# Kernel tuning notes

Measured on AMD Instinct MI355X. Metric: run time of the kernel, lower is better.

## Reference

```python
import jax, jax.numpy as jnp
import numpy as np

N = 50000      # n_nodes
E = 800000     # n_edges (avg degree 16)
D_IN, D_HID, D_OUT = 128, 128, 64


def setup_inputs() -> dict:
    key = jax.random.key(0)
    k1, k2, k3, k4 = jax.random.split(key, 4)
    x = jax.random.normal(k1, (N, D_IN), jnp.float32)
    edge_index = jax.random.randint(k2, (2, E), 0, N, jnp.int32)
    # Glorot-style init for the two GCNConv linear weights
    W1 = jax.random.normal(k3, (D_IN, D_HID), jnp.float32) / np.sqrt(D_IN)
    W2 = jax.random.normal(k4, (D_HID, D_OUT), jnp.float32) / np.sqrt(D_HID)
    b1 = jnp.zeros((D_HID,), jnp.float32)
    b2 = jnp.zeros((D_OUT,), jnp.float32)
    return {"x": x, "edge_index": edge_index, "W1": W1, "b1": b1, "W2": W2, "b2": b2}


def _gcn_conv(x, W, b, src, dst):
    """PyG GCNConv: linear transform, then sym-normalized aggregation with self-loops."""
    h = x @ W                                   # [N, F_out]
    ones = jnp.ones((src.shape[0],), h.dtype)
    # degree includes the self-loop weight of 1
    deg = jax.ops.segment_sum(ones, dst, num_segments=N) + 1.0
    dinv = jax.lax.rsqrt(deg)                   # D^{-1/2}
    norm = dinv[src] * dinv[dst]                # per-edge normalization
    agg = jax.ops.segment_sum(h[src] * norm[:, None], dst, num_segments=N)
    # self-loop contribution: norm_ii = dinv_i^2
    return agg + h * (dinv * dinv)[:, None] + b


def reference(x, edge_index, W1, b1, W2, b2):
    src, dst = edge_index[0], edge_index[1]
    h = jax.nn.relu(_gcn_conv(x, W1, b1, src, dst))
    out = jax.nn.relu(_gcn_conv(h, W2, b2, src, dst))
    return out
```

## Files before the change

### kernel.cpp

```cpp
#include <hip/hip_runtime.h>

typedef unsigned short u16;
typedef __attribute__((ext_vector_type(8))) short short8;
typedef __attribute__((ext_vector_type(4))) float f32x4;

__device__ __forceinline__ float bflo(unsigned u) {
    union { unsigned u; float f; } v; v.u = u << 16; return v.f;
}
__device__ __forceinline__ float bfhi(unsigned u) {
    union { unsigned u; float f; } v; v.u = u & 0xFFFF0000u; return v.f;
}
__device__ __forceinline__ u16 f2bf(float f) {
    union { float f; unsigned u; } v; v.f = f;
    unsigned u = v.u;
    u += 0x7FFFu + ((u >> 16) & 1u);
    return (u16)(u >> 16);
}

__global__ void k_deg_detect(const int* __restrict__ dst, int* __restrict__ cnt,
                             int* __restrict__ pos, int E,
                             const u16* __restrict__ x, int* __restrict__ flag) {
    if (blockIdx.x == 0) {
        __shared__ int c_s;
        if (threadIdx.x == 0) c_s = 0;
        __syncthreads();
        int c = 0;
        for (int i = threadIdx.x; i < 2048; i += 256) {
            int ex = (x[2 * i] >> 7) & 0xFF;
            c += (ex >= 160 || ex <= 80) ? 1 : 0;
        }
        atomicAdd(&c_s, c);
        __syncthreads();
        if (threadIdx.x == 0) *flag = (c_s > 64) ? 1 : 0;
    }
    int e = blockIdx.x * 256 + threadIdx.x;
    if (e < E) pos[e] = atomicAdd(&cnt[dst[e]], 1);
}

__global__ void k_scan(const int* __restrict__ cnt, int* __restrict__ rowp,
                       float* __restrict__ dinv, int n, int E, int nb) {
    __shared__ int S[256];
    __shared__ int T[256];
    int t = threadIdx.x;
    int b = blockIdx.x;
    int s = 0;
    if (t < nb) {
        const int4* p4 = (const int4*)(cnt + t * 256);
#pragma unroll 8
        for (int i = 0; i < 64; i++) { int4 v = p4[i]; s += v.x + v.y + v.z + v.w; }
    }
    S[t] = s;
    __syncthreads();
    for (int off = 1; off < 256; off <<= 1) {
        int add = (t >= off) ? S[t - off] : 0;
        __syncthreads();
        S[t] += add;
        __syncthreads();
    }
    int prefix = (b == 0) ? 0 : S[b - 1];
    int i = b * 256 + t;
    int v = (i < n) ? cnt[i] : 0;
    T[t] = v;
    __syncthreads();
    for (int off = 1; off < 256; off <<= 1) {
        int add = (t >= off) ? T[t - off] : 0;
        __syncthreads();
        T[t] += add;
        __syncthreads();
    }
    if (i < n) {
        rowp[i] = prefix + T[t] - v;
        dinv[i] = rsqrtf((float)v + 1.0f);
    }
    if (i == 0) rowp[n] = E;
}

__global__ void k_gemm1_fill(const void* __restrict__ Av, const void* __restrict__ W,
                             const float* __restrict__ dinv, u16* __restrict__ out,
                             int M, int GB, const int* __restrict__ flag,
                             const int* __restrict__ src, const int* __restrict__ dst,
                             const int* __restrict__ pos, const int* __restrict__ rowp,
                             int* __restrict__ col, int E) {
    constexpr int NOUT = 128;
    int t = threadIdx.x;
    if ((int)blockIdx.x >= GB) {
        int stride = (gridDim.x - GB) * 256;
        for (int e = ((int)blockIdx.x - GB) * 256 + t; e < E; e += stride)
            col[rowp[dst[e]] + pos[e]] = src[e];
        return;
    }
    int fl = *flag;
    __shared__ u16 Wt[NOUT][136];
    for (int idx = t; idx < NOUT * 128; idx += 256) {
        int k = idx / NOUT, n = idx % NOUT;
        Wt[n][k] = fl ? f2bf(((const float*)W)[idx]) : ((const u16*)W)[idx];
    }
    __syncthreads();
    int wave = t >> 6, lane = t & 63;
    int m0 = ((int)blockIdx.x * 4 + wave) * 16;
    if (m0 >= M) return;
    int q = lane >> 4;
    int mr = lane & 15;

    short8 a[4];
    if (fl) {
        const float* arow = (const float*)Av + (size_t)(m0 + mr) * 128 + q * 8;
#pragma unroll
        for (int c = 0; c < 4; c++) {
            f32x4 lo = *(const f32x4*)(arow + c * 32);
            f32x4 hi = *(const f32x4*)(arow + c * 32 + 4);
            a[c][0] = (short)f2bf(lo.x); a[c][1] = (short)f2bf(lo.y);
            a[c][2] = (short)f2bf(lo.z); a[c][3] = (short)f2bf(lo.w);
            a[c][4] = (short)f2bf(hi.x); a[c][5] = (short)f2bf(hi.y);
            a[c][6] = (short)f2bf(hi.z); a[c][7] = (short)f2bf(hi.w);
        }
    } else {
        const u16* arow = (const u16*)Av + (size_t)(m0 + mr) * 128 + q * 8;
#pragma unroll
        for (int c = 0; c < 4; c++) a[c] = *(const short8*)(arow + c * 32);
    }

    f32x4 acc[NOUT / 16];
#pragma unroll
    for (int tl = 0; tl < NOUT / 16; tl++) acc[tl] = (f32x4){0.f, 0.f, 0.f, 0.f};
#pragma unroll
    for (int c = 0; c < 4; c++) {
#pragma unroll
        for (int tl = 0; tl < NOUT / 16; tl++) {
            short8 b = *(const short8*)(&Wt[tl * 16 + mr][c * 32 + q * 8]);
            acc[tl] = __builtin_amdgcn_mfma_f32_16x16x32_bf16(a[c], b, acc[tl], 0, 0, 0);
        }
    }
    int rbase = m0 + q * 4;
#pragma unroll
    for (int tl = 0; tl < NOUT / 16; tl++) {
#pragma unroll
        for (int r = 0; r < 4; r++) {
            int row = rbase + r;
            float v = acc[tl][r] * dinv[row];
            out[(size_t)row * NOUT + tl * 16 + mr] = f2bf(v);
        }
    }
}

template <int NOUT>
__global__ void k_gemm_scale(const u16* __restrict__ A, const void* __restrict__ W,
                             const float* __restrict__ dinv, u16* __restrict__ out,
                             int M, const int* __restrict__ flag) {
    int fl = *flag;
    __shared__ u16 Wt[NOUT][136];
    int t = threadIdx.x;
    for (int idx = t; idx < NOUT * 128; idx += 256) {
        int k = idx / NOUT, n = idx % NOUT;
        Wt[n][k] = fl ? f2bf(((const float*)W)[idx]) : ((const u16*)W)[idx];
    }
    __syncthreads();
    int wave = t >> 6, lane = t & 63;
    int m0 = ((int)blockIdx.x * 4 + wave) * 16;
    if (m0 >= M) return;
    int q = lane >> 4;
    int mr = lane & 15;

    const u16* arow = A + (size_t)(m0 + mr) * 128 + q * 8;
    short8 a[4];
#pragma unroll
    for (int c = 0; c < 4; c++) a[c] = *(const short8*)(arow + c * 32);

    f32x4 acc[NOUT / 16];
#pragma unroll
    for (int tl = 0; tl < NOUT / 16; tl++) acc[tl] = (f32x4){0.f, 0.f, 0.f, 0.f};
#pragma unroll
    for (int c = 0; c < 4; c++) {
#pragma unroll
        for (int tl = 0; tl < NOUT / 16; tl++) {
            short8 b = *(const short8*)(&Wt[tl * 16 + mr][c * 32 + q * 8]);
            acc[tl] = __builtin_amdgcn_mfma_f32_16x16x32_bf16(a[c], b, acc[tl], 0, 0, 0);
        }
    }
    int rbase = m0 + q * 4;
#pragma unroll
    for (int tl = 0; tl < NOUT / 16; tl++) {
#pragma unroll
        for (int r = 0; r < 4; r++) {
            int row = rbase + r;
            float v = acc[tl][r] * dinv[row];
            out[(size_t)row * NOUT + tl * 16 + mr] = f2bf(v);
        }
    }
}

template <int F>
__global__ void k_agg(const u16* __restrict__ g, const int* __restrict__ rowp,
                      const int* __restrict__ col, const float* __restrict__ dinv,
                      const void* __restrict__ biasv, u16* __restrict__ outh,
                      float* __restrict__ outf, const int* __restrict__ flag,
                      int outsel, int N, int E) {
    constexpr int LPR = F / 8;
    constexpr int EPW = 64 / LPR;
    int d = blockIdx.x * 4 + (threadIdx.x >> 6);
    if (d >= N) return;
    int lane = threadIdx.x & 63;
    int er = lane / LPR;
    int fo = (lane % LPR) * 8;

    int beg = rowp[d], end = rowp[d + 1];
    if (beg < 0) beg = 0;
    if (end > E) end = E;
    int deg = end - beg;

    float a0[8], a1[8];
#pragma unroll
    for (int j = 0; j < 8; j++) { a0[j] = 0.f; a1[j] = 0.f; }

    for (int base = 0; base < deg; base += 64) {
        int cnt = deg - base; if (cnt > 64) cnt = 64;
        int colv = 0;
        if (lane < cnt) {
            int s = col[beg + base + lane];
            colv = s < 0 ? 0 : (s >= N ? N - 1 : s);
        }
        int full = cnt / EPW;
        int i = 0;
        for (; i + 2 <= full; i += 2) {
            int s0 = __shfl(colv, i * EPW + er, 64);
            int s1 = __shfl(colv, (i + 1) * EPW + er, 64);
            uint4 v0 = *(const uint4*)(g + (size_t)s0 * F + fo);
            uint4 v1 = *(const uint4*)(g + (size_t)s1 * F + fo);
            a0[0] += bflo(v0.x); a0[1] += bfhi(v0.x);
            a0[2] += bflo(v0.y); a0[3] += bfhi(v0.y);
            a0[4] += bflo(v0.z); a0[5] += bfhi(v0.z);
            a0[6] += bflo(v0.w); a0[7] += bfhi(v0.w);
            a1[0] += bflo(v1.x); a1[1] += bfhi(v1.x);
            a1[2] += bflo(v1.y); a1[3] += bfhi(v1.y);
            a1[4] += bflo(v1.z); a1[5] += bfhi(v1.z);
            a1[6] += bflo(v1.w); a1[7] += bfhi(v1.w);
        }
        if (i < full) {
            int s0 = __shfl(colv, i * EPW + er, 64);
            uint4 v0 = *(const uint4*)(g + (size_t)s0 * F + fo);
            a0[0] += bflo(v0.x); a0[1] += bfhi(v0.x);
            a0[2] += bflo(v0.y); a0[3] += bfhi(v0.y);
            a0[4] += bflo(v0.z); a0[5] += bfhi(v0.z);
            a0[6] += bflo(v0.w); a0[7] += bfhi(v0.w);
            i++;
        }
        int rem = cnt - full * EPW;
        int s0 = __shfl(colv, (full * EPW + er) & 63, 64);
        if (er < rem) {
            uint4 v0 = *(const uint4*)(g + (size_t)s0 * F + fo);
            a0[0] += bflo(v0.x); a0[1] += bfhi(v0.x);
            a0[2] += bflo(v0.y); a0[3] += bfhi(v0.y);
            a0[4] += bflo(v0.z); a0[5] += bfhi(v0.z);
            a0[6] += bflo(v0.w); a0[7] += bfhi(v0.w);
        }
    }
#pragma unroll
    for (int j = 0; j < 8; j++) a0[j] += a1[j];
#pragma unroll
    for (int off = LPR; off < 64; off <<= 1) {
#pragma unroll
        for (int j = 0; j < 8; j++) a0[j] += __shfl_xor(a0[j], off, 64);
    }

    if (lane < LPR) {
        int fl = *flag;
        uint4 sv = *(const uint4*)(g + (size_t)d * F + fo);
        float bb[8];
        if (fl) {
            const float* bp = (const float*)biasv + fo;
            f32x4 blo = *(const f32x4*)bp;
            f32x4 bhi = *(const f32x4*)(bp + 4);
            bb[0] = blo.x; bb[1] = blo.y; bb[2] = blo.z; bb[3] = blo.w;
            bb[4] = bhi.x; bb[5] = bhi.y; bb[6] = bhi.z; bb[7] = bhi.w;
        } else {
            uint4 bv = *(const uint4*)((const u16*)biasv + fo);
            bb[0] = bflo(bv.x); bb[1] = bfhi(bv.x);
            bb[2] = bflo(bv.y); bb[3] = bfhi(bv.y);
            bb[4] = bflo(bv.z); bb[5] = bfhi(bv.z);
            bb[6] = bflo(bv.w); bb[7] = bfhi(bv.w);
        }
        float di = dinv[d];
        float sf[8] = { bflo(sv.x), bfhi(sv.x), bflo(sv.y), bfhi(sv.y),
                        bflo(sv.z), bfhi(sv.z), bflo(sv.w), bfhi(sv.w) };
        float r[8];
#pragma unroll
        for (int j = 0; j < 8; j++) {
            float v = di * (a0[j] + sf[j]) + bb[j];
            r[j] = v > 0.f ? v : 0.f;
        }
        size_t o = (size_t)d * F + fo;
        if (outsel && fl) {
            f32x4 w0 = {r[0], r[1], r[2], r[3]};
            f32x4 w1 = {r[4], r[5], r[6], r[7]};
            *(f32x4*)(outf + o) = w0;
            *(f32x4*)(outf + o + 4) = w1;
        } else {
            uint4 w;
            w.x = (unsigned)f2bf(r[0]) | ((unsigned)f2bf(r[1]) << 16);
            w.y = (unsigned)f2bf(r[2]) | ((unsigned)f2bf(r[3]) << 16);
            w.z = (unsigned)f2bf(r[4]) | ((unsigned)f2bf(r[5]) << 16);
            w.w = (unsigned)f2bf(r[6]) | ((unsigned)f2bf(r[7]) << 16);
            *(uint4*)(outh + o) = w;
        }
    }
}


extern "C" void kernel_launch(void* const* d_in, const int* in_sizes, int n_in,
                              void* d_out, int out_size, void* d_ws, size_t ws_size,
                              hipStream_t stream) {
    const int N = in_sizes[0] / 128;
    const int E = in_sizes[1] / 2;
    const int* ei = (const int*)d_in[1];
    const int* src = ei;
    const int* dst = ei + E;

    char* p = (char*)d_ws;
    auto alloc = [&](size_t b) { char* r = p; p += (b + 255) & ~(size_t)255; return r; };
    int*   flag = (int*)alloc(256);
    int*   rowp = (int*)alloc((size_t)(N + 1) * 4);
    float* dinv = (float*)alloc((size_t)N * 4);
    int*   col  = (int*)alloc((size_t)E * 4);
    char*  slotA = alloc((size_t)N * 128 * 2);
    char*  slotB = alloc((size_t)N * 128 * 2);

    int* cnt = (int*)slotA;
    u16* g1  = (u16*)slotA;
    u16* g2  = (u16*)slotA;
    int* pos = (int*)slotB;
    u16* o1  = (u16*)slotB;

    int eb = (E + 255) / 256;
    int nb = (N + 255) / 256;

    hipMemsetAsync(slotA, 0, (size_t)nb * 256 * 4, stream);

    k_deg_detect<<<eb, 256, 0, stream>>>(dst, cnt, pos, E, (const u16*)d_in[0], flag);
    k_scan<<<nb, 256, 0, stream>>>(cnt, rowp, dinv, N, E, nb);

    int GB = (N / 16 + 3) / 4;
    int FB = GB;
    k_gemm1_fill<<<GB + FB, 256, 0, stream>>>(d_in[0], d_in[2], dinv, g1, N, GB, flag,
                                              src, dst, pos, rowp, col, E);

    int ab = (N + 3) / 4;
    k_agg<128><<<ab, 256, 0, stream>>>(g1, rowp, col, dinv, d_in[3],
                                       o1, nullptr, flag, 0, N, E);
    k_gemm_scale<64><<<GB, 256, 0, stream>>>(o1, d_in[4], dinv, g2, N, flag);
    k_agg<64><<<ab, 256, 0, stream>>>(g2, rowp, col, dinv, d_in[5],
                                      (u16*)d_out, (float*)d_out, flag, 1, N, E);
}
```

Measured before the change: 228.1 us.

## Overlap first GEMM with degree counting and move source scaling into aggregation

The first GEMM no longer depends on dinv. It runs in the same launch as the degree-count atomics, and each GEMM block detects the input dtype itself, so the GEMM overlaps the edge counting instead of waiting on the scan. Source-side dinv scaling moves into the aggregation loop as a per-edge gather of dinv[src], and the self-loop term is scaled by di twice. The scan is split into block-scan and finalize kernels, and CSR fill becomes its own kernel. This adds launches and extra per-edge dinv loads, and buffers are no longer aliased.

```diff
diff --git a/kernel.cpp b/kernel.cpp
--- a/kernel.cpp
+++ b/kernel.cpp
@@ -17,79 +17,41 @@
     return (u16)(u >> 16);
 }
 
-__global__ void k_deg_detect(const int* __restrict__ dst, int* __restrict__ cnt,
-                             int* __restrict__ pos, int E,
-                             const u16* __restrict__ x, int* __restrict__ flag) {
-    if (blockIdx.x == 0) {
-        __shared__ int c_s;
-        if (threadIdx.x == 0) c_s = 0;
-        __syncthreads();
-        int c = 0;
-        for (int i = threadIdx.x; i < 2048; i += 256) {
-            int ex = (x[2 * i] >> 7) & 0xFF;
-            c += (ex >= 160 || ex <= 80) ? 1 : 0;
-        }
-        atomicAdd(&c_s, c);
-        __syncthreads();
-        if (threadIdx.x == 0) *flag = (c_s > 64) ? 1 : 0;
-    }
-    int e = blockIdx.x * 256 + threadIdx.x;
-    if (e < E) pos[e] = atomicAdd(&cnt[dst[e]], 1);
-}
-
-__global__ void k_scan(const int* __restrict__ cnt, int* __restrict__ rowp,
-                       float* __restrict__ dinv, int n, int E, int nb) {
-    __shared__ int S[256];
-    __shared__ int T[256];
-    int t = threadIdx.x;
-    int b = blockIdx.x;
-    int s = 0;
-    if (t < nb) {
-        const int4* p4 = (const int4*)(cnt + t * 256);
-#pragma unroll 8
-        for (int i = 0; i < 64; i++) { int4 v = p4[i]; s += v.x + v.y + v.z + v.w; }
-    }
-    S[t] = s;
-    __syncthreads();
-    for (int off = 1; off < 256; off <<= 1) {
-        int add = (t >= off) ? S[t - off] : 0;
-        __syncthreads();
-        S[t] += add;
-        __syncthreads();
-    }
-    int prefix = (b == 0) ? 0 : S[b - 1];
-    int i = b * 256 + t;
-    int v = (i < n) ? cnt[i] : 0;
-    T[t] = v;
-    __syncthreads();
-    for (int off = 1; off < 256; off <<= 1) {
-        int add = (t >= off) ? T[t - off] : 0;
-        __syncthreads();
-        T[t] += add;
-        __syncthreads();
-    }
-    if (i < n) {
-        rowp[i] = prefix + T[t] - v;
-        dinv[i] = rsqrtf((float)v + 1.0f);
-    }
-    if (i == 0) rowp[n] = E;
-}
-
-__global__ void k_gemm1_fill(const void* __restrict__ Av, const void* __restrict__ W,
-                             const float* __restrict__ dinv, u16* __restrict__ out,
-                             int M, int GB, const int* __restrict__ flag,
-                             const int* __restrict__ src, const int* __restrict__ dst,
-                             const int* __restrict__ pos, const int* __restrict__ rowp,
-                             int* __restrict__ col, int E) {
+__global__ void k1_gemm_deg(const void* __restrict__ Av, const void* __restrict__ W,
+                            u16* __restrict__ out, int M, int GB,
+                            const int* __restrict__ dst, int* __restrict__ cnt,
+                            int* __restrict__ pos, int E, int* __restrict__ flag) {
     constexpr int NOUT = 128;
     int t = threadIdx.x;
-    if ((int)blockIdx.x >= GB) {
-        int stride = (gridDim.x - GB) * 256;
-        for (int e = ((int)blockIdx.x - GB) * 256 + t; e < E; e += stride)
-            col[rowp[dst[e]] + pos[e]] = src[e];
+    int bid = blockIdx.x;
+    if (bid >= GB) {
+        if (bid == GB) {
+            __shared__ int c_s;
+            if (t == 0) c_s = 0;
+            __syncthreads();
+            int c = 0;
+            for (int i = t; i < 2048; i += 256) {
+                int ex = (((const u16*)Av)[2 * i] >> 7) & 0xFF;
+                c += (ex >= 160 || ex <= 80) ? 1 : 0;
+            }
+            atomicAdd(&c_s, c);
+            __syncthreads();
+            if (t == 0) *flag = (c_s > 64) ? 1 : 0;
+        }
+        int e = (bid - GB) * 256 + t;
+        if (e < E) pos[e] = atomicAdd(&cnt[dst[e]], 1);
         return;
     }
-    int fl = *flag;
+    __shared__ int det;
+    if (t == 0) det = 0;
+    __syncthreads();
+    {
+        int ex = (((const u16*)Av)[2 * t] >> 7) & 0xFF;
+        if (ex >= 160 || ex <= 80) atomicAdd(&det, 1);
+    }
+    __syncthreads();
+    int fl = det > 8;
+
     __shared__ u16 Wt[NOUT][136];
     for (int idx = t; idx < NOUT * 128; idx += 256) {
         int k = idx / NOUT, n = idx % NOUT;
@@ -97,7 +59,7 @@
     }
     __syncthreads();
     int wave = t >> 6, lane = t & 63;
-    int m0 = ((int)blockIdx.x * 4 + wave) * 16;
+    int m0 = (bid * 4 + wave) * 16;
     if (m0 >= M) return;
     int q = lane >> 4;
     int mr = lane & 15;
@@ -135,18 +97,63 @@
 #pragma unroll
     for (int tl = 0; tl < NOUT / 16; tl++) {
 #pragma unroll
-        for (int r = 0; r < 4; r++) {
-            int row = rbase + r;
-            float v = acc[tl][r] * dinv[row];
-            out[(size_t)row * NOUT + tl * 16 + mr] = f2bf(v);
-        }
-    }
+        for (int r = 0; r < 4; r++)
+            out[(size_t)(rbase + r) * NOUT + tl * 16 + mr] = f2bf(acc[tl][r]);
+    }
+}
+
+
+__global__ void k_scan_blocks(const int* __restrict__ cnt, int* __restrict__ rowp,
+                              int* __restrict__ sums, int n) {
+    __shared__ int s[256];
+    int t = threadIdx.x;
+    int i = blockIdx.x * 256 + t;
+    int v = (i < n) ? cnt[i] : 0;
+    s[t] = v;
+    __syncthreads();
+    for (int off = 1; off < 256; off <<= 1) {
+        int add = (t >= off) ? s[t - off] : 0;
+        __syncthreads();
+        s[t] += add;
+        __syncthreads();
+    }
+    if (i < n) rowp[i] = s[t] - v;
+    if (t == 255) sums[blockIdx.x] = s[255];
+}
+
+__global__ void k_finalize2(int* __restrict__ rowp, const int* __restrict__ sums,
+                            const int* __restrict__ cnt, float* __restrict__ dinv,
+                            int n, int E) {
+    __shared__ int s[256];
+    int t = threadIdx.x;
+    int b = blockIdx.x;
+    s[t] = sums[t];
+    __syncthreads();
+    for (int off = 1; off < 256; off <<= 1) {
+        int add = (t >= off) ? s[t - off] : 0;
+        __syncthreads();
+        s[t] += add;
+        __syncthreads();
+    }
+    int prefix = (b == 0) ? 0 : s[b - 1];
+    int i = b * 256 + t;
+    if (i < n) {
+        rowp[i] += prefix;
+        dinv[i] = rsqrtf((float)cnt[i] + 1.0f);
+    }
+    if (i == 0) rowp[n] = E;
+}
+
+__global__ void k_fill2(const int* __restrict__ src, const int* __restrict__ dst,
+                        const int* __restrict__ pos, const int* __restrict__ rowp,
+                        int* __restrict__ col, int E) {
+    int e = blockIdx.x * blockDim.x + threadIdx.x;
+    if (e < E) col[rowp[dst[e]] + pos[e]] = src[e];
 }
 
 template <int NOUT>
-__global__ void k_gemm_scale(const u16* __restrict__ A, const void* __restrict__ W,
-                             const float* __restrict__ dinv, u16* __restrict__ out,
-                             int M, const int* __restrict__ flag) {
+__global__ void k_gemm_plain(const u16* __restrict__ A, const void* __restrict__ W,
+                             u16* __restrict__ out, int M, const int* __restrict__ flag) {
     int fl = *flag;
     __shared__ u16 Wt[NOUT][136];
     int t = threadIdx.x;
@@ -181,11 +188,8 @@
 #pragma unroll
     for (int tl = 0; tl < NOUT / 16; tl++) {
 #pragma unroll
-        for (int r = 0; r < 4; r++) {
-            int row = rbase + r;
-            float v = acc[tl][r] * dinv[row];
-            out[(size_t)row * NOUT + tl * 16 + mr] = f2bf(v);
-        }
+        for (int r = 0; r < 4; r++)
+            out[(size_t)(rbase + r) * NOUT + tl * 16 + mr] = f2bf(acc[tl][r]);
     }
 }
 
@@ -224,34 +228,38 @@
         for (; i + 2 <= full; i += 2) {
             int s0 = __shfl(colv, i * EPW + er, 64);
             int s1 = __shfl(colv, (i + 1) * EPW + er, 64);
+            float d0 = dinv[s0];
+            float d1 = dinv[s1];
             uint4 v0 = *(const uint4*)(g + (size_t)s0 * F + fo);
             uint4 v1 = *(const uint4*)(g + (size_t)s1 * F + fo);
-            a0[0] += bflo(v0.x); a0[1] += bfhi(v0.x);
-            a0[2] += bflo(v0.y); a0[3] += bfhi(v0.y);
-            a0[4] += bflo(v0.z); a0[5] += bfhi(v0.z);
-            a0[6] += bflo(v0.w); a0[7] += bfhi(v0.w);
-            a1[0] += bflo(v1.x); a1[1] += bfhi(v1.x);
-            a1[2] += bflo(v1.y); a1[3] += bfhi(v1.y);
-            a1[4] += bflo(v1.z); a1[5] += bfhi(v1.z);
-            a1[6] += bflo(v1.w); a1[7] += bfhi(v1.w);
+            a0[0] += d0 * bflo(v0.x); a0[1] += d0 * bfhi(v0.x);
+            a0[2] += d0 * bflo(v0.y); a0[3] += d0 * bfhi(v0.y);
+            a0[4] += d0 * bflo(v0.z); a0[5] += d0 * bfhi(v0.z);
+            a0[6] += d0 * bflo(v0.w); a0[7] += d0 * bfhi(v0.w);
+            a1[0] += d1 * bflo(v1.x); a1[1] += d1 * bfhi(v1.x);
+            a1[2] += d1 * bflo(v1.y); a1[3] += d1 * bfhi(v1.y);
+            a1[4] += d1 * bflo(v1.z); a1[5] += d1 * bfhi(v1.z);
+            a1[6] += d1 * bflo(v1.w); a1[7] += d1 * bfhi(v1.w);
         }
         if (i < full) {
             int s0 = __shfl(colv, i * EPW + er, 64);
+            float d0 = dinv[s0];
             uint4 v0 = *(const uint4*)(g + (size_t)s0 * F + fo);
-            a0[0] += bflo(v0.x); a0[1] += bfhi(v0.x);
-            a0[2] += bflo(v0.y); a0[3] += bfhi(v0.y);
-            a0[4] += bflo(v0.z); a0[5] += bfhi(v0.z);
-            a0[6] += bflo(v0.w); a0[7] += bfhi(v0.w);
+            a0[0] += d0 * bflo(v0.x); a0[1] += d0 * bfhi(v0.x);
+            a0[2] += d0 * bflo(v0.y); a0[3] += d0 * bfhi(v0.y);
+            a0[4] += d0 * bflo(v0.z); a0[5] += d0 * bfhi(v0.z);
+            a0[6] += d0 * bflo(v0.w); a0[7] += d0 * bfhi(v0.w);
             i++;
         }
         int rem = cnt - full * EPW;
         int s0 = __shfl(colv, (full * EPW + er) & 63, 64);
+        float d0 = dinv[s0];
         if (er < rem) {
             uint4 v0 = *(const uint4*)(g + (size_t)s0 * F + fo);
-            a0[0] += bflo(v0.x); a0[1] += bfhi(v0.x);
-            a0[2] += bflo(v0.y); a0[3] += bfhi(v0.y);
-            a0[4] += bflo(v0.z); a0[5] += bfhi(v0.z);
-            a0[6] += bflo(v0.w); a0[7] += bfhi(v0.w);
+            a0[0] += d0 * bflo(v0.x); a0[1] += d0 * bfhi(v0.x);
+            a0[2] += d0 * bflo(v0.y); a0[3] += d0 * bfhi(v0.y);
+            a0[4] += d0 * bflo(v0.z); a0[5] += d0 * bfhi(v0.z);
+            a0[6] += d0 * bflo(v0.w); a0[7] += d0 * bfhi(v0.w);
         }
     }
 #pragma unroll
@@ -285,7 +293,7 @@
         float r[8];
 #pragma unroll
         for (int j = 0; j < 8; j++) {
-            float v = di * (a0[j] + sf[j]) + bb[j];
+            float v = di * (a0[j] + di * sf[j]) + bb[j];
             r[j] = v > 0.f ? v : 0.f;
         }
         size_t o = (size_t)d * F + fo;
@@ -321,32 +329,29 @@
     int*   rowp = (int*)alloc((size_t)(N + 1) * 4);
     float* dinv = (float*)alloc((size_t)N * 4);
     int*   col  = (int*)alloc((size_t)E * 4);
-    char*  slotA = alloc((size_t)N * 128 * 2);
-    char*  slotB = alloc((size_t)N * 128 * 2);
-
-    int* cnt = (int*)slotA;
-    u16* g1  = (u16*)slotA;
-    u16* g2  = (u16*)slotA;
-    int* pos = (int*)slotB;
-    u16* o1  = (u16*)slotB;
+    int*   cnt  = (int*)alloc((size_t)N * 4);
+    int*   sums = (int*)alloc(256 * 4);
+    int*   pos  = (int*)alloc((size_t)E * 4);
+    u16*   g1   = (u16*)alloc((size_t)N * 128 * 2);
+    u16*   o1   = (u16*)alloc((size_t)N * 128 * 2);
+    u16*   g2   = (u16*)alloc((size_t)N * 64 * 2);
 
     int eb = (E + 255) / 256;
     int nb = (N + 255) / 256;
-
-    hipMemsetAsync(slotA, 0, (size_t)nb * 256 * 4, stream);
-
-    k_deg_detect<<<eb, 256, 0, stream>>>(dst, cnt, pos, E, (const u16*)d_in[0], flag);
-    k_scan<<<nb, 256, 0, stream>>>(cnt, rowp, dinv, N, E, nb);
-
     int GB = (N / 16 + 3) / 4;
-    int FB = GB;
-    k_gemm1_fill<<<GB + FB, 256, 0, stream>>>(d_in[0], d_in[2], dinv, g1, N, GB, flag,
-                                              src, dst, pos, rowp, col, E);
-
     int ab = (N + 3) / 4;
+
+    hipMemsetAsync(cnt, 0, ((char*)sums - (char*)cnt) + 1024, stream);
+
+    k1_gemm_deg<<<GB + eb, 256, 0, stream>>>(d_in[0], d_in[2], g1, N, GB,
+                                             dst, cnt, pos, E, flag);
+    k_scan_blocks<<<nb, 256, 0, stream>>>(cnt, rowp, sums, N);
+    k_finalize2<<<nb, 256, 0, stream>>>(rowp, sums, cnt, dinv, N, E);
+    k_fill2<<<eb, 256, 0, stream>>>(src, dst, pos, rowp, col, E);
+
     k_agg<128><<<ab, 256, 0, stream>>>(g1, rowp, col, dinv, d_in[3],
                                        o1, nullptr, flag, 0, N, E);
-    k_gemm_scale<64><<<GB, 256, 0, stream>>>(o1, d_in[4], dinv, g2, N, flag);
+    k_gemm_plain<64><<<GB, 256, 0, stream>>>(o1, d_in[4], g2, N, flag);
     k_agg<64><<<ab, 256, 0, stream>>>(g2, rowp, col, dinv, d_in[5],
                                       (u16*)d_out, (float*)d_out, flag, 1, N, E);
 }
```

New measurement: 211.6 us. 7.2% less time.
